# Kernel tuning notes

Measured on AMD Instinct MI355X. Metric: run time of the kernel, lower is better.

Reference implementation:

```python
import jax, jax.numpy as jnp
import numpy as np

DIM, HEADS, FFN, E = 1024, 16, 4096, 8
B, S = 2, 1024
EPS = 1e-5


def _ln(x, g, b):
    mu = jnp.mean(x, axis=-1, keepdims=True)
    var = jnp.mean((x - mu) ** 2, axis=-1, keepdims=True)
    return (x - mu) * jax.lax.rsqrt(var + EPS) * g + b


def setup_inputs() -> dict:
    key = jax.random.key(0)
    ks = jax.random.split(key, 20)
    sd = 0.02
    d, f = DIM, FFN
    return {
        "x": jax.random.normal(ks[0], (B, S, d), jnp.float32),
        "ln1_g": jnp.ones((d,), jnp.float32), "ln1_b": jnp.zeros((d,), jnp.float32),
        "Wqkv": jax.random.normal(ks[1], (d, 3 * d), jnp.float32) * sd,
        "bqkv": jnp.zeros((3 * d,), jnp.float32),
        "Wo": jax.random.normal(ks[2], (d, d), jnp.float32) * sd,
        "bo": jnp.zeros((d,), jnp.float32),
        "ln2_g": jnp.ones((d,), jnp.float32), "ln2_b": jnp.zeros((d,), jnp.float32),
        "gate_w": jax.random.normal(ks[3], (d, E), jnp.float32) * sd,
        "W1": jax.random.normal(ks[4], (E, d, f), jnp.float32) * sd,
        "b1": jnp.zeros((E, f), jnp.float32),
        "W2": jax.random.normal(ks[5], (E, f, d), jnp.float32) * sd,
        "b2": jnp.zeros((E, d), jnp.float32),
        "rW1": jax.random.normal(ks[6], (d, f), jnp.float32) * sd,
        "rb1": jnp.zeros((f,), jnp.float32),
        "rW2": jax.random.normal(ks[7], (f, d), jnp.float32) * sd,
        "rb2": jnp.zeros((d,), jnp.float32),
        "coef_w": jax.random.normal(ks[8], (d, 2), jnp.float32) * sd,
        "coef_b": jnp.zeros((2,), jnp.float32),
    }


def reference(x, ln1_g, ln1_b, Wqkv, bqkv, Wo, bo, ln2_g, ln2_b, gate_w,
              W1, b1, W2, b2, rW1, rb1, rW2, rb2, coef_w, coef_b):
    b, s, d = x.shape
    h, dh = HEADS, d // HEADS

    # --- attention block ---
    xn = _ln(x, ln1_g, ln1_b)
    qkv = xn @ Wqkv + bqkv                       # [b,s,3d]
    q, k, v = jnp.split(qkv, 3, axis=-1)
    q = q.reshape(b, s, h, dh)
    k = k.reshape(b, s, h, dh)
    v = v.reshape(b, s, h, dh)
    scores = jnp.einsum("bqhd,bkhd->bhqk", q, k) / jnp.sqrt(jnp.float32(dh))
    attn = jax.nn.softmax(scores, axis=-1)
    ctx = jnp.einsum("bhqk,bkhd->bqhd", attn, v).reshape(b, s, d)
    x = x + ctx @ Wo + bo

    # --- MoE FFN block (top-1 gating, DeepSpeed residual MoE) ---
    xn2 = _ln(x, ln2_g, ln2_b)
    xt = xn2.reshape(b * s, d)                   # [T,d] tokens
    probs = jax.nn.softmax(xt @ gate_w, axis=-1)  # [T,E]
    gate_val = jnp.max(probs, axis=-1, keepdims=True)   # top-1 prob
    expert_idx = jnp.argmax(probs, axis=-1)
    oh = jax.nn.one_hot(expert_idx, E, dtype=xt.dtype)  # [T,E] dispatch mask

    xe = jnp.einsum("te,td->etd", oh, xt)        # dispatch [E,T,d]
    he = jax.nn.gelu(jnp.einsum("etd,edf->etf", xe, W1) + b1[:, None, :], approximate=False)
    ye = jnp.einsum("etf,efd->etd", he, W2) + b2[:, None, :]
    moe_out = jnp.einsum("te,etd->td", oh, ye) * gate_val  # combine [T,d]

    # residual dense expert + learned mixing coefficient
    rm = jax.nn.gelu(xt @ rW1 + rb1, approximate=False) @ rW2 + rb2
    coef = jax.nn.softmax(xt @ coef_w + coef_b, axis=-1)  # [T,2]
    ff = moe_out * coef[:, 0:1] + rm * coef[:, 1:2]

    return x + ff.reshape(b, s, d)
```

## Files before the change

### kernel.cpp

```cpp
#include <hip/hip_runtime.h>
#include <math.h>

#define TOK 2048
#define NDIM 1024

typedef __attribute__((ext_vector_type(4))) float f32x4;
typedef __attribute__((ext_vector_type(8))) short s16x8;
typedef __attribute__((ext_vector_type(4))) short s16x4;

__device__ __forceinline__ short f2bf(float x) {
  unsigned int u = __builtin_bit_cast(unsigned int, x);
  unsigned int r = (u + 0x7fffu + ((u >> 16) & 1u)) >> 16;
  return (short)r;
}
__device__ __forceinline__ void gload_lds16(const void* g, void* l) {
  __builtin_amdgcn_global_load_lds((const __attribute__((address_space(1))) void*)g,
                                   (__attribute__((address_space(3))) void*)l, 16, 0, 0);
}

struct PackP { const float* src; short* dst; int K, N, nkt; };
__global__ __launch_bounds__(256)
void pack_k(PackP p)
{
  __shared__ short T[64][264];
  const int nkt = p.nkt;
  const int cb = blockIdx.x / nkt, kt = blockIdx.x % nkt;
  const int ntn = p.N >> 7;
  const float* src = p.src + (size_t)blockIdx.y * p.K * p.N + (size_t)(kt * 64) * p.N + cb * 256;
  const int t = threadIdx.x;
  #pragma unroll
  for (int i = 0; i < 16; ++i) {
    const int r = i * 4 + (t >> 6);
    const f32x4 v = *(const f32x4*)(src + (size_t)r * p.N + (t & 63) * 4);
    short* d = &T[r][(t & 63) * 4];
    d[0] = f2bf(v[0]); d[1] = f2bf(v[1]); d[2] = f2bf(v[2]); d[3] = f2bf(v[3]);
  }
  __syncthreads();
  #pragma unroll
  for (int j = 0; j < 2; ++j) {
    short* dst = p.dst + ((size_t)(blockIdx.y * ntn + cb * 2 + j) * nkt + kt) * 8192;
    #pragma unroll
    for (int jj = 0; jj < 4; ++jj) {
      const int ch = t * 4 + jj;
      const int col = ch >> 3, od = ch & 7, o = od ^ (col & 7);
      s16x8 v;
      #pragma unroll
      for (int kk = 0; kk < 8; ++kk) v[kk] = T[o * 8 + kk][j * 128 + col];
      *(s16x8*)(dst + ch * 8) = v;
    }
  }
}

__global__ __launch_bounds__(256)
void ln_k(const float* __restrict__ x, const float* __restrict__ g,
          const float* __restrict__ bb, short* __restrict__ out)
{
  const int row = blockIdx.x, tid = threadIdx.x;
  const f32x4 xv = *(const f32x4*)(x + (size_t)row * NDIM + tid * 4);
  float s = xv[0] + xv[1] + xv[2] + xv[3];
  float s2 = xv[0]*xv[0] + xv[1]*xv[1] + xv[2]*xv[2] + xv[3]*xv[3];
  #pragma unroll
  for (int m = 1; m < 64; m <<= 1) { s += __shfl_xor(s, m); s2 += __shfl_xor(s2, m); }
  __shared__ float red[8];
  const int w = tid >> 6, l = tid & 63;
  if (l == 0) { red[w] = s; red[4 + w] = s2; }
  __syncthreads();
  s = red[0] + red[1] + red[2] + red[3];
  s2 = red[4] + red[5] + red[6] + red[7];
  const float mean = s * (1.0f / NDIM);
  const float var = s2 * (1.0f / NDIM) - mean * mean;
  const float rstd = rsqrtf(var + 1e-5f);
  const f32x4 gv = *(const f32x4*)(g + tid * 4);
  const f32x4 bv = *(const f32x4*)(bb + tid * 4);
  s16x4 ov;
  #pragma unroll
  for (int j = 0; j < 4; ++j) ov[j] = f2bf((xv[j] - mean) * rstd * gv[j] + bv[j]);
  *(s16x4*)(out + (size_t)row * NDIM + tid * 4) = ov;
}

__global__ __launch_bounds__(256)
void gate_k(const float* __restrict__ x1, const float* __restrict__ g,
            const float* __restrict__ bb, const float* __restrict__ gw,
            const float* __restrict__ cw, const float* __restrict__ cb,
            int* __restrict__ counts, int* __restrict__ bucket,
            float* __restrict__ gs, float* __restrict__ c1o)
{
  const int tid = threadIdx.x, l = tid & 63, w = tid >> 6;
  const int t = blockIdx.x * 4 + w;
  f32x4 xv[4];
  #pragma unroll
  for (int it = 0; it < 4; ++it)
    xv[it] = *(const f32x4*)(x1 + (size_t)t * NDIM + it * 256 + l * 4);
  float s = 0.f, s2 = 0.f;
  #pragma unroll
  for (int it = 0; it < 4; ++it)
    #pragma unroll
    for (int j = 0; j < 4; ++j) { s += xv[it][j]; s2 += xv[it][j] * xv[it][j]; }
  #pragma unroll
  for (int m = 1; m < 64; m <<= 1) { s += __shfl_xor(s, m); s2 += __shfl_xor(s2, m); }
  const float mean = s * (1.0f / NDIM);
  const float rstd = rsqrtf(s2 * (1.0f / NDIM) - mean * mean + 1e-5f);
  float acc[10];
  #pragma unroll
  for (int j = 0; j < 10; ++j) acc[j] = 0.f;
  #pragma unroll
  for (int it = 0; it < 4; ++it) {
    #pragma unroll
    for (int j = 0; j < 4; ++j) {
      const int d0 = it * 256 + l * 4 + j;
      const float xn = (xv[it][j] - mean) * rstd * g[d0] + bb[d0];
      const f32x4 g0 = *(const f32x4*)(gw + (size_t)d0 * 8);
      const f32x4 g1 = *(const f32x4*)(gw + (size_t)d0 * 8 + 4);
      #pragma unroll
      for (int q = 0; q < 4; ++q) { acc[q] += xn * g0[q]; acc[4 + q] += xn * g1[q]; }
      acc[8] += xn * cw[d0 * 2]; acc[9] += xn * cw[d0 * 2 + 1];
    }
  }
  #pragma unroll
  for (int j = 0; j < 10; ++j)
    #pragma unroll
    for (int m = 1; m < 64; m <<= 1) acc[j] += __shfl_xor(acc[j], m);
  if (l == 0) {
    int best = 0; float mx = acc[0];
    #pragma unroll
    for (int e = 1; e < 8; ++e) if (acc[e] > mx) { mx = acc[e]; best = e; }
    float se = 0.f;
    #pragma unroll
    for (int e = 0; e < 8; ++e) se += __expf(acc[e] - mx);
    const float gate_val = 1.0f / se;
    const float l0 = acc[8] + cb[0], l1 = acc[9] + cb[1];
    const float cmx = fmaxf(l0, l1);
    const float e0 = __expf(l0 - cmx), e1 = __expf(l1 - cmx);
    const float inv = 1.0f / (e0 + e1);
    const int pos = atomicAdd(&counts[best], 1);
    bucket[best * TOK + pos] = t;
    gs[t] = gate_val * e0 * inv;
    c1o[t] = e1 * inv;
  }
}

struct GemmP {
  const short* A; const short* A2; const short* Bp; const short* Bp2;
  const float* bias; const float* bias2;
  short* outh; short* outh2; float* outf;
  const float* resid; const float* gs; const float* c1;
  const int* bucket; const int* counts;
  int N, K, ktc, nmt;
};

template<int MODE>
__global__ __launch_bounds__(256, 3)
void gemm_k(GemmP p)
{
  __shared__ short Al[8192];
  __shared__ short Bl[8192];
  const int tid = threadIdx.x;
  const int l = tid & 63, w = tid >> 6;
  const int wr = w >> 1, wc = w & 1;
  const int ntn = p.N >> 7, nkt = p.K >> 6;
  const int nwg = p.nmt * ntn;
  const int logical = (blockIdx.x & 7) * (nwg >> 3) + (blockIdx.x >> 3);
  const int nt = logical / p.nmt;
  const int mt = logical % p.nmt;
  const int z = blockIdx.z;
  const bool first = (z == 0);
  const int K = p.K, N = p.N;

  int e = 0, cnt = TOK;
  const int* bucket = nullptr;
  if (MODE >= 2) {
    e = blockIdx.y;
    if (e < 8) {
      cnt = p.counts[e];
      if (mt * 128 >= cnt) return;
      bucket = p.bucket + e * TOK;
    }
  }
  const short* Abase = (MODE == 3 && e == 8) ? p.A2 : p.A;
  const float* bias = (MODE >= 2) ? (e < 8 ? p.bias + (size_t)e * N : p.bias2) : p.bias;
  const short* btile = (MODE >= 2)
      ? (e < 8 ? p.Bp + ((size_t)(e * ntn + nt) * nkt) * 8192
               : p.Bp2 + ((size_t)nt * nkt) * 8192)
      : p.Bp + ((size_t)nt * nkt) * 8192;

  const short* aptr[4];
  #pragma unroll
  for (int i = 0; i < 4; ++i) {
    const int rl = (i * 256 + tid) >> 3;
    int row;
    if (bucket) {
      const int bidx = mt * 128 + rl;
      row = bucket[bidx < cnt ? bidx : mt * 128];
    } else row = mt * 128 + rl;
    aptr[i] = Abase + (size_t)row * K + ((tid & 7) ^ (rl & 7)) * 8;
  }

  const int kt0 = z * p.ktc, kt1 = kt0 + p.ktc;

  f32x4 acc[4][4] = {};
  for (int kt = kt0; kt < kt1; ++kt) {
    const short* bsrc = btile + kt * 8192;
    #pragma unroll
    for (int j = 0; j < 4; ++j)
      gload_lds16(bsrc + (j * 256 + tid) * 8, (char*)Bl + (j * 256 + (tid & 192)) * 16);
    #pragma unroll
    for (int i = 0; i < 4; ++i)
      gload_lds16(aptr[i] + kt * 64, (char*)Al + (i * 256 + (tid & 192)) * 16);
    __syncthreads();
    #pragma unroll
    for (int ks = 0; ks < 2; ++ks) {
      const int octd = (ks * 4 + (l >> 4)) ^ (l & 7);
      s16x8 af[4], bfr[4];
      #pragma unroll
      for (int mf = 0; mf < 4; ++mf)
        af[mf] = *(const s16x8*)((char*)Al +
            (wr * 64 + mf * 16 + (l & 15)) * 128 + octd * 16);
      #pragma unroll
      for (int nf = 0; nf < 4; ++nf)
        bfr[nf] = *(const s16x8*)((char*)Bl +
            (wc * 64 + nf * 16 + (l & 15)) * 128 + octd * 16);
      #pragma unroll
      for (int mf = 0; mf < 4; ++mf)
        #pragma unroll
        for (int nf = 0; nf < 4; ++nf)
          acc[mf][nf] = __builtin_amdgcn_mfma_f32_16x16x32_bf16(af[mf], bfr[nf], acc[mf][nf], 0, 0, 0);
    }
    __syncthreads();
  }

  short* oh = (MODE == 2) ? (e < 8 ? p.outh : p.outh2) : p.outh;
  #pragma unroll
  for (int mf = 0; mf < 4; ++mf) {
    #pragma unroll
    for (int i = 0; i < 4; ++i) {
      const int rloc = wr * 64 + mf * 16 + (l >> 4) * 4 + i;
      int grow; bool valid = true;
      if (bucket) {
        const int bidx = mt * 128 + rloc;
        valid = bidx < cnt;
        grow = valid ? bucket[bidx] : 0;
      } else grow = mt * 128 + rloc;
      float srow = 1.f;
      if (MODE == 3) srow = (e < 8) ? (valid ? p.gs[grow] : 0.f) : p.c1[grow];
      #pragma unroll
      for (int nf = 0; nf < 4; ++nf) {
        const int col = nt * 128 + wc * 64 + nf * 16 + (l & 15);
        const size_t off = (size_t)grow * N + col;
        const float bc = first ? bias[col] : 0.f;
        if (MODE == 0) {
          oh[off] = f2bf(acc[mf][nf][i] + bc);
        } else if (MODE == 1) {
          atomicAdd(&p.outf[off], acc[mf][nf][i] + bc + (first ? p.resid[off] : 0.f));
        } else if (MODE == 2) {
          const float v = acc[mf][nf][i] + bc;
          const float gv = 0.5f * v * (1.0f + erff(v * 0.70710678f));
          if (valid) oh[off] = f2bf(gv);
        } else if (MODE == 3) {
          if (valid)
            atomicAdd(&p.outf[off], (acc[mf][nf][i] + bc) * srow +
                      ((e == 8 && first) ? p.resid[off] : 0.f));
        }
      }
    }
  }
}

__global__ __launch_bounds__(256, 2)
void attn_k(const short* __restrict__ qkv, short* __restrict__ ctx)
{
  __shared__ short Klds[64 * 64];
  __shared__ short Vlds[64 * 64];
  __shared__ short Plds[4 * 16 * 64];
  const int tid = threadIdx.x, l = tid & 63, w = tid >> 6;
  const int qt = blockIdx.x;
  const int bh = blockIdx.y;
  const int b = bh >> 4, h = bh & 15;
  const size_t tbase = (size_t)b * 1024;

  const int sq = qt * 64 + w * 16 + (l & 15);
  s16x8 qf[2];
  #pragma unroll
  for (int ks = 0; ks < 2; ++ks)
    qf[ks] = *(const s16x8*)(qkv + (tbase + sq) * 3072 + h * 64 + ks * 32 + (l >> 4) * 8);

  f32x4 o[4] = {};
  float mrow[4], lrow[4];
  #pragma unroll
  for (int i = 0; i < 4; ++i) { mrow[i] = -1e30f; lrow[i] = 0.f; }

  for (int kt = 0; kt < 16; ++kt) {
    #pragma unroll
    for (int i = 0; i < 2; ++i) {
      const int s = i * 256 + tid;
      const int r = s >> 3, c = s & 7, csrc = c ^ (r & 7);
      const short* gsrc = qkv + (tbase + kt * 64 + r) * 3072 + 1024 + h * 64 + csrc * 8;
      gload_lds16(gsrc, (char*)Klds + (i * 256 + (tid & 192)) * 16);
    }
    #pragma unroll
    for (int i = 0; i < 2; ++i) {
      const int kv0 = (i * 4 + w) * 8;
      s16x8 vv;
      #pragma unroll
      for (int j = 0; j < 8; ++j)
        vv[j] = qkv[(tbase + kt * 64 + kv0 + j) * 3072 + 2048 + h * 64 + l];
      *(s16x8*)((char*)Vlds + ((l * 128 + kv0 * 2) ^ ((l & 7) << 4))) = vv;
    }
    __syncthreads();

    f32x4 sv[4];
    #pragma unroll
    for (int nf = 0; nf < 4; ++nf) {
      f32x4 a = {0.f, 0.f, 0.f, 0.f};
      const int kv = nf * 16 + (l & 15);
      #pragma unroll
      for (int ks = 0; ks < 2; ++ks) {
        const s16x8 kb = *(const s16x8*)((char*)Klds +
            ((kv * 128 + (ks * 32 + (l >> 4) * 8) * 2) ^ ((kv & 7) << 4)));
        a = __builtin_amdgcn_mfma_f32_16x16x32_bf16(qf[ks], kb, a, 0, 0, 0);
      }
      sv[nf] = a * 0.125f;
    }
    float sc[4], ps[4];
    #pragma unroll
    for (int i = 0; i < 4; ++i) {
      float m = fmaxf(fmaxf(sv[0][i], sv[1][i]), fmaxf(sv[2][i], sv[3][i]));
      #pragma unroll
      for (int msk = 1; msk < 16; msk <<= 1) m = fmaxf(m, __shfl_xor(m, msk));
      const float mn = fmaxf(mrow[i], m);
      sc[i] = __expf(mrow[i] - mn);
      mrow[i] = mn;
      ps[i] = 0.f;
    }
    #pragma unroll
    for (int nf = 0; nf < 4; ++nf)
      #pragma unroll
      for (int i = 0; i < 4; ++i) {
        const float pp = __expf(sv[nf][i] - mrow[i]);
        sv[nf][i] = pp;
        ps[i] += pp;
      }
    #pragma unroll
    for (int i = 0; i < 4; ++i) {
      #pragma unroll
      for (int msk = 1; msk < 16; msk <<= 1) ps[i] += __shfl_xor(ps[i], msk);
      lrow[i] = lrow[i] * sc[i] + ps[i];
    }
    #pragma unroll
    for (int nf = 0; nf < 4; ++nf)
      #pragma unroll
      for (int i = 0; i < 4; ++i) o[nf][i] *= sc[i];

    char* pw = (char*)Plds + w * 2048;
    #pragma unroll
    for (int nf = 0; nf < 4; ++nf)
      #pragma unroll
      for (int i = 0; i < 4; ++i) {
        const int q = (l >> 4) * 4 + i;
        *(short*)(pw + ((q * 128 + (nf * 16 + (l & 15)) * 2) ^ ((q & 7) << 4))) = f2bf(sv[nf][i]);
      }
    __syncthreads();
    #pragma unroll
    for (int ks = 0; ks < 2; ++ks) {
      const s16x8 pa = *(const s16x8*)(pw +
          (((l & 15) * 128 + (ks * 32 + (l >> 4) * 8) * 2) ^ ((l & 7) << 4)));
      #pragma unroll
      for (int nf = 0; nf < 4; ++nf) {
        const int dh = nf * 16 + (l & 15);
        const s16x8 vb = *(const s16x8*)((char*)Vlds +
            ((dh * 128 + (ks * 32 + (l >> 4) * 8) * 2) ^ ((dh & 7) << 4)));
        o[nf] = __builtin_amdgcn_mfma_f32_16x16x32_bf16(pa, vb, o[nf], 0, 0, 0);
      }
    }
    __syncthreads();
  }
  #pragma unroll
  for (int i = 0; i < 4; ++i) {
    const float inv = 1.0f / lrow[i];
    const size_t t = tbase + qt * 64 + w * 16 + (l >> 4) * 4 + i;
    #pragma unroll
    for (int nf = 0; nf < 4; ++nf)
      ctx[t * 1024 + h * 64 + nf * 16 + (l & 15)] = f2bf(o[nf][i] * inv);
  }
}

extern "C" void kernel_launch(void* const* d_in, const int* in_sizes, int n_in,
                              void* d_out, int out_size, void* d_ws, size_t ws_size,
                              hipStream_t stream)
{
  const float* x    = (const float*)d_in[0];
  const float* ln1g = (const float*)d_in[1];
  const float* ln1b = (const float*)d_in[2];
  const float* Wqkv = (const float*)d_in[3];
  const float* bqkv = (const float*)d_in[4];
  const float* Wo   = (const float*)d_in[5];
  const float* bo   = (const float*)d_in[6];
  const float* ln2g = (const float*)d_in[7];
  const float* ln2b = (const float*)d_in[8];
  const float* gw   = (const float*)d_in[9];
  const float* W1   = (const float*)d_in[10];
  const float* b1   = (const float*)d_in[11];
  const float* W2   = (const float*)d_in[12];
  const float* b2   = (const float*)d_in[13];
  const float* rW1  = (const float*)d_in[14];
  const float* rb1  = (const float*)d_in[15];
  const float* rW2  = (const float*)d_in[16];
  const float* rb2  = (const float*)d_in[17];
  const float* cw   = (const float*)d_in[18];
  const float* cb   = (const float*)d_in[19];
  float* out = (float*)d_out;

  char* ws = (char*)d_ws;
  const size_t MB = 1024 * 1024;
  short* xn1    = (short*)(ws + 0);
  short* qkv    = (short*)(ws + 4 * MB);
  short* he     = (short*)(ws + 4 * MB);
  short* ctx    = (short*)(ws + 16 * MB);
  float* x1     = (float*)(ws + 20 * MB);
  short* xn2    = (short*)(ws + 28 * MB);
  short* hr     = (short*)(ws + 32 * MB);
  int*   counts = (int*)(ws + 56 * MB);
  int*   bucket = (int*)(ws + 56 * MB + 256);
  float* gs     = (float*)(ws + 56 * MB + 256 + 64 * 1024);
  float* c1     = (float*)(ws + 56 * MB + 256 + 64 * 1024 + 8192);
  short* Wqkvp  = (short*)(ws + 64 * MB);
  short* Wop    = (short*)(ws + 70 * MB);
  short* W1p    = (short*)(ws + 72 * MB);
  short* W2p    = (short*)(ws + 136 * MB);
  short* rW1p   = (short*)(ws + 200 * MB);
  short* rW2p   = (short*)(ws + 208 * MB);

  hipMemsetAsync(counts, 0, 8 * sizeof(int), stream);
  hipMemsetAsync(x1, 0, TOK * NDIM * sizeof(float), stream);
  hipMemsetAsync(out, 0, TOK * NDIM * sizeof(float), stream);

  PackP pk;
  pk = PackP{Wqkv, Wqkvp, 1024, 3072, 16}; pack_k<<<dim3(12 * 16, 1), 256, 0, stream>>>(pk);
  pk = PackP{Wo,   Wop,   1024, 1024, 16}; pack_k<<<dim3(4 * 16, 1), 256, 0, stream>>>(pk);
  pk = PackP{W1,   W1p,   1024, 4096, 16}; pack_k<<<dim3(16 * 16, 8), 256, 0, stream>>>(pk);
  pk = PackP{W2,   W2p,   4096, 1024, 64}; pack_k<<<dim3(4 * 64, 8), 256, 0, stream>>>(pk);
  pk = PackP{rW1,  rW1p,  1024, 4096, 16}; pack_k<<<dim3(16 * 16, 1), 256, 0, stream>>>(pk);
  pk = PackP{rW2,  rW2p,  4096, 1024, 64}; pack_k<<<dim3(4 * 64, 1), 256, 0, stream>>>(pk);

  ln_k<<<TOK, 256, 0, stream>>>(x, ln1g, ln1b, xn1);

  GemmP p{};
  p.A = xn1; p.Bp = Wqkvp; p.bias = bqkv; p.outh = qkv;
  p.N = 3072; p.K = 1024; p.ktc = 16; p.nmt = 16;
  gemm_k<0><<<dim3(384), 256, 0, stream>>>(p);

  attn_k<<<dim3(16, 32), 256, 0, stream>>>(qkv, ctx);

  p = GemmP{};
  p.A = ctx; p.Bp = Wop; p.bias = bo; p.outf = x1; p.resid = x;
  p.N = 1024; p.K = 1024; p.ktc = 8; p.nmt = 16;
  gemm_k<1><<<dim3(128, 1, 2), 256, 0, stream>>>(p);

  ln_k<<<TOK, 256, 0, stream>>>(x1, ln2g, ln2b, xn2);
  gate_k<<<TOK / 4, 256, 0, stream>>>(x1, ln2g, ln2b, gw, cw, cb, counts, bucket, gs, c1);

  p = GemmP{};
  p.A = xn2; p.Bp = W1p; p.Bp2 = rW1p; p.bias = b1; p.bias2 = rb1;
  p.outh = he; p.outh2 = hr; p.N = 4096; p.K = 1024; p.ktc = 16; p.nmt = 16;
  p.bucket = bucket; p.counts = counts;
  gemm_k<2><<<dim3(512, 9), 256, 0, stream>>>(p);

  p = GemmP{};
  p.A = he; p.A2 = hr; p.Bp = W2p; p.Bp2 = rW2p; p.bias = b2; p.bias2 = rb2;
  p.outf = out; p.resid = x1; p.gs = gs; p.c1 = c1;
  p.N = 1024; p.K = 4096; p.ktc = 32; p.nmt = 16;
  p.bucket = bucket; p.counts = counts;
  gemm_k<3><<<dim3(128, 9, 2), 256, 0, stream>>>(p);
}
```

Before: 500.5 us.

## Add 256x256 double-buffered GEMM kernel for MoE expert FFN layers

Adds a new 512-thread GEMM kernel with 256x256 output tiles and double-buffered LDS staging (prefetching the next k-tile while computing the current one) for the expert and residual FFN GEMMs. The weight packing gains a wide 256-column tile format to match. The original kernel is simplified to the dense modes only. The intent is more data reuse per tile and overlap of global loads with MFMA work. The cost is lower occupancy (one block per CU, large LDS), more wasted rows for sparsely filled expert buckets at 256-row granularity, and fewer workgroups overall.

```diff
diff --git a/kernel.cpp b/kernel.cpp
--- a/kernel.cpp
+++ b/kernel.cpp
@@ -18,14 +18,13 @@
                                    (__attribute__((address_space(3))) void*)l, 16, 0, 0);
 }
 
-struct PackP { const float* src; short* dst; int K, N, nkt; };
+struct PackP { const float* src; short* dst; int K, N, nkt, wide; };
 __global__ __launch_bounds__(256)
 void pack_k(PackP p)
 {
   __shared__ short T[64][264];
   const int nkt = p.nkt;
   const int cb = blockIdx.x / nkt, kt = blockIdx.x % nkt;
-  const int ntn = p.N >> 7;
   const float* src = p.src + (size_t)blockIdx.y * p.K * p.N + (size_t)(kt * 64) * p.N + cb * 256;
   const int t = threadIdx.x;
   #pragma unroll
@@ -36,17 +35,32 @@
     d[0] = f2bf(v[0]); d[1] = f2bf(v[1]); d[2] = f2bf(v[2]); d[3] = f2bf(v[3]);
   }
   __syncthreads();
-  #pragma unroll
-  for (int j = 0; j < 2; ++j) {
-    short* dst = p.dst + ((size_t)(blockIdx.y * ntn + cb * 2 + j) * nkt + kt) * 8192;
-    #pragma unroll
-    for (int jj = 0; jj < 4; ++jj) {
-      const int ch = t * 4 + jj;
+  if (p.wide) {
+    const int ntn = p.N >> 8;
+    short* dst = p.dst + ((size_t)(blockIdx.y * ntn + cb) * nkt + kt) * 16384;
+    #pragma unroll
+    for (int jj = 0; jj < 8; ++jj) {
+      const int ch = t * 8 + jj;
       const int col = ch >> 3, od = ch & 7, o = od ^ (col & 7);
       s16x8 v;
       #pragma unroll
-      for (int kk = 0; kk < 8; ++kk) v[kk] = T[o * 8 + kk][j * 128 + col];
+      for (int kk = 0; kk < 8; ++kk) v[kk] = T[o * 8 + kk][col];
       *(s16x8*)(dst + ch * 8) = v;
+    }
+  } else {
+    const int ntn = p.N >> 7;
+    #pragma unroll
+    for (int j = 0; j < 2; ++j) {
+      short* dst = p.dst + ((size_t)(blockIdx.y * ntn + cb * 2 + j) * nkt + kt) * 8192;
+      #pragma unroll
+      for (int jj = 0; jj < 4; ++jj) {
+        const int ch = t * 4 + jj;
+        const int col = ch >> 3, od = ch & 7, o = od ^ (col & 7);
+        s16x8 v;
+        #pragma unroll
+        for (int kk = 0; kk < 8; ++kk) v[kk] = T[o * 8 + kk][j * 128 + col];
+        *(s16x8*)(dst + ch * 8) = v;
+      }
     }
   }
 }
@@ -165,38 +179,18 @@
   const int z = blockIdx.z;
   const bool first = (z == 0);
   const int K = p.K, N = p.N;
-
-  int e = 0, cnt = TOK;
-  const int* bucket = nullptr;
-  if (MODE >= 2) {
-    e = blockIdx.y;
-    if (e < 8) {
-      cnt = p.counts[e];
-      if (mt * 128 >= cnt) return;
-      bucket = p.bucket + e * TOK;
-    }
-  }
-  const short* Abase = (MODE == 3 && e == 8) ? p.A2 : p.A;
-  const float* bias = (MODE >= 2) ? (e < 8 ? p.bias + (size_t)e * N : p.bias2) : p.bias;
-  const short* btile = (MODE >= 2)
-      ? (e < 8 ? p.Bp + ((size_t)(e * ntn + nt) * nkt) * 8192
-               : p.Bp2 + ((size_t)nt * nkt) * 8192)
-      : p.Bp + ((size_t)nt * nkt) * 8192;
+  const short* btile = p.Bp + ((size_t)nt * nkt) * 8192;
+  const float* bias = p.bias;
 
   const short* aptr[4];
   #pragma unroll
   for (int i = 0; i < 4; ++i) {
     const int rl = (i * 256 + tid) >> 3;
-    int row;
-    if (bucket) {
-      const int bidx = mt * 128 + rl;
-      row = bucket[bidx < cnt ? bidx : mt * 128];
-    } else row = mt * 128 + rl;
-    aptr[i] = Abase + (size_t)row * K + ((tid & 7) ^ (rl & 7)) * 8;
+    const int row = mt * 128 + rl;
+    aptr[i] = p.A + (size_t)row * K + ((tid & 7) ^ (rl & 7)) * 8;
   }
 
   const int kt0 = z * p.ktc, kt1 = kt0 + p.ktc;
-
   f32x4 acc[4][4] = {};
   for (int kt = kt0; kt < kt1; ++kt) {
     const short* bsrc = btile + kt * 8192;
@@ -209,16 +203,18 @@
     __syncthreads();
     #pragma unroll
     for (int ks = 0; ks < 2; ++ks) {
-      const int octd = (ks * 4 + (l >> 4)) ^ (l & 7);
+      const int octd0 = ks * 4 + (l >> 4);
       s16x8 af[4], bfr[4];
       #pragma unroll
-      for (int mf = 0; mf < 4; ++mf)
-        af[mf] = *(const s16x8*)((char*)Al +
-            (wr * 64 + mf * 16 + (l & 15)) * 128 + octd * 16);
-      #pragma unroll
-      for (int nf = 0; nf < 4; ++nf)
-        bfr[nf] = *(const s16x8*)((char*)Bl +
-            (wc * 64 + nf * 16 + (l & 15)) * 128 + octd * 16);
+      for (int mf = 0; mf < 4; ++mf) {
+        const int r = wr * 64 + mf * 16 + (l & 15);
+        af[mf] = *(const s16x8*)((char*)Al + r * 128 + (octd0 ^ (r & 7)) * 16);
+      }
+      #pragma unroll
+      for (int nf = 0; nf < 4; ++nf) {
+        const int c2 = wc * 64 + nf * 16 + (l & 15);
+        bfr[nf] = *(const s16x8*)((char*)Bl + c2 * 128 + (octd0 ^ (c2 & 7)) * 16);
+      }
       #pragma unroll
       for (int mf = 0; mf < 4; ++mf)
         #pragma unroll
@@ -228,36 +224,142 @@
     __syncthreads();
   }
 
-  short* oh = (MODE == 2) ? (e < 8 ? p.outh : p.outh2) : p.outh;
   #pragma unroll
   for (int mf = 0; mf < 4; ++mf) {
     #pragma unroll
     for (int i = 0; i < 4; ++i) {
-      const int rloc = wr * 64 + mf * 16 + (l >> 4) * 4 + i;
-      int grow; bool valid = true;
-      if (bucket) {
-        const int bidx = mt * 128 + rloc;
-        valid = bidx < cnt;
-        grow = valid ? bucket[bidx] : 0;
-      } else grow = mt * 128 + rloc;
-      float srow = 1.f;
-      if (MODE == 3) srow = (e < 8) ? (valid ? p.gs[grow] : 0.f) : p.c1[grow];
+      const int grow = mt * 128 + wr * 64 + mf * 16 + (l >> 4) * 4 + i;
       #pragma unroll
       for (int nf = 0; nf < 4; ++nf) {
         const int col = nt * 128 + wc * 64 + nf * 16 + (l & 15);
         const size_t off = (size_t)grow * N + col;
         const float bc = first ? bias[col] : 0.f;
         if (MODE == 0) {
-          oh[off] = f2bf(acc[mf][nf][i] + bc);
-        } else if (MODE == 1) {
+          p.outh[off] = f2bf(acc[mf][nf][i] + bc);
+        } else {
           atomicAdd(&p.outf[off], acc[mf][nf][i] + bc + (first ? p.resid[off] : 0.f));
-        } else if (MODE == 2) {
-          const float v = acc[mf][nf][i] + bc;
+        }
+      }
+    }
+  }
+}
+
+template<int MODE>
+__global__ __launch_bounds__(512, 1)
+void gemm256_k(GemmP p)
+{
+  __shared__ short Al[2][16384];
+  __shared__ short Bl[2][16384];
+  const int tid = threadIdx.x;
+  const int l = tid & 63, wid = tid >> 6;
+  const int wr = wid >> 2, wc = wid & 3;
+  const int ntn = p.N >> 8, nkt = p.K >> 6;
+  const int nwg = p.nmt * ntn;
+  const int logical = (blockIdx.x & 7) * (nwg >> 3) + (blockIdx.x >> 3);
+  const int nt = logical / p.nmt;
+  const int mt = logical % p.nmt;
+  const int z = blockIdx.z;
+  const bool first = (z == 0);
+  const int K = p.K, N = p.N;
+
+  const int e = blockIdx.y;
+  int cnt = TOK;
+  const int* bucket = nullptr;
+  if (e < 8) {
+    cnt = p.counts[e];
+    if (mt * 256 >= cnt) return;
+    bucket = p.bucket + e * TOK;
+  }
+  const short* Abase = (MODE == 3 && e == 8) ? p.A2 : p.A;
+  const float* bias = (e < 8) ? p.bias + (size_t)e * N : p.bias2;
+  const short* btile = (e < 8) ? p.Bp + ((size_t)(e * ntn + nt) * nkt) * 16384
+                               : p.Bp2 + ((size_t)nt * nkt) * 16384;
+
+  const short* aptr[4];
+  #pragma unroll
+  for (int i = 0; i < 4; ++i) {
+    const int rl = (i * 512 + tid) >> 3;
+    int row;
+    if (bucket) {
+      const int bidx = mt * 256 + rl;
+      row = bucket[bidx < cnt ? bidx : mt * 256];
+    } else row = mt * 256 + rl;
+    aptr[i] = Abase + (size_t)row * K + ((tid & 7) ^ (rl & 7)) * 8;
+  }
+
+  auto stage = [&](int kt, int buf) {
+    const short* bsrc = btile + (size_t)kt * 16384;
+    #pragma unroll
+    for (int i = 0; i < 4; ++i)
+      gload_lds16(aptr[i] + kt * 64, (char*)Al[buf] + (i * 512 + (tid & 448)) * 16);
+    #pragma unroll
+    for (int i = 0; i < 4; ++i)
+      gload_lds16(bsrc + (i * 512 + tid) * 8, (char*)Bl[buf] + (i * 512 + (tid & 448)) * 16);
+  };
+
+  const int kt0 = z * p.ktc, kt1 = kt0 + p.ktc;
+  f32x4 acc[8][4] = {};
+  stage(kt0, 0);
+  __syncthreads();
+  for (int kt = kt0; kt < kt1; ++kt) {
+    const int cur = (kt - kt0) & 1;
+    if (kt + 1 < kt1) stage(kt + 1, cur ^ 1);
+    __builtin_amdgcn_s_setprio(1);
+    #pragma unroll
+    for (int ks = 0; ks < 2; ++ks) {
+      const int octd0 = ks * 4 + (l >> 4);
+      s16x8 bfr[4];
+      #pragma unroll
+      for (int nf = 0; nf < 4; ++nf) {
+        const int c2 = wc * 64 + nf * 16 + (l & 15);
+        bfr[nf] = *(const s16x8*)((char*)Bl[cur] + c2 * 128 + (octd0 ^ (c2 & 7)) * 16);
+      }
+      #pragma unroll
+      for (int mfh = 0; mfh < 2; ++mfh) {
+        s16x8 af[4];
+        #pragma unroll
+        for (int mf = 0; mf < 4; ++mf) {
+          const int r = wr * 128 + mfh * 64 + mf * 16 + (l & 15);
+          af[mf] = *(const s16x8*)((char*)Al[cur] + r * 128 + (octd0 ^ (r & 7)) * 16);
+        }
+        #pragma unroll
+        for (int mf = 0; mf < 4; ++mf)
+          #pragma unroll
+          for (int nf = 0; nf < 4; ++nf)
+            acc[mfh * 4 + mf][nf] =
+                __builtin_amdgcn_mfma_f32_16x16x32_bf16(af[mf], bfr[nf], acc[mfh * 4 + mf][nf], 0, 0, 0);
+      }
+    }
+    __builtin_amdgcn_s_setprio(0);
+    __syncthreads();
+  }
+
+  short* oh = (e < 8) ? p.outh : p.outh2;
+  #pragma unroll
+  for (int m8 = 0; m8 < 8; ++m8) {
+    #pragma unroll
+    for (int i = 0; i < 4; ++i) {
+      const int rloc = wr * 128 + (m8 >> 2) * 64 + (m8 & 3) * 16 + (l >> 4) * 4 + i;
+      int grow; bool valid = true;
+      if (bucket) {
+        const int bidx = mt * 256 + rloc;
+        valid = bidx < cnt;
+        grow = valid ? bucket[bidx] : 0;
+      } else grow = mt * 256 + rloc;
+      float srow = 1.f;
+      if (MODE == 3) srow = (e < 8) ? (valid ? p.gs[grow] : 0.f) : p.c1[grow];
+      #pragma unroll
+      for (int nf = 0; nf < 4; ++nf) {
+        const int col = nt * 256 + wc * 64 + nf * 16 + (l & 15);
+        const size_t off = (size_t)grow * N + col;
+        const float bc = first ? bias[col] : 0.f;
+        if (MODE == 2) {
+          const float v = acc[m8][nf][i] + bc;
           const float gv = 0.5f * v * (1.0f + erff(v * 0.70710678f));
           if (valid) oh[off] = f2bf(gv);
-        } else if (MODE == 3) {
+        } else {
           if (valid)
-            atomicAdd(&p.outf[off], (acc[mf][nf][i] + bc) * srow +
+            atomicAdd(&p.outf[off], (acc[m8][nf][i] + bc) * srow +
                       ((e == 8 && first) ? p.resid[off] : 0.f));
         }
       }
@@ -434,12 +536,12 @@
   hipMemsetAsync(out, 0, TOK * NDIM * sizeof(float), stream);
 
   PackP pk;
-  pk = PackP{Wqkv, Wqkvp, 1024, 3072, 16}; pack_k<<<dim3(12 * 16, 1), 256, 0, stream>>>(pk);
-  pk = PackP{Wo,   Wop,   1024, 1024, 16}; pack_k<<<dim3(4 * 16, 1), 256, 0, stream>>>(pk);
-  pk = PackP{W1,   W1p,   1024, 4096, 16}; pack_k<<<dim3(16 * 16, 8), 256, 0, stream>>>(pk);
-  pk = PackP{W2,   W2p,   4096, 1024, 64}; pack_k<<<dim3(4 * 64, 8), 256, 0, stream>>>(pk);
-  pk = PackP{rW1,  rW1p,  1024, 4096, 16}; pack_k<<<dim3(16 * 16, 1), 256, 0, stream>>>(pk);
-  pk = PackP{rW2,  rW2p,  4096, 1024, 64}; pack_k<<<dim3(4 * 64, 1), 256, 0, stream>>>(pk);
+  pk = PackP{Wqkv, Wqkvp, 1024, 3072, 16, 0}; pack_k<<<dim3(12 * 16, 1), 256, 0, stream>>>(pk);
+  pk = PackP{Wo,   Wop,   1024, 1024, 16, 0}; pack_k<<<dim3(4 * 16, 1), 256, 0, stream>>>(pk);
+  pk = PackP{W1,   W1p,   1024, 4096, 16, 1}; pack_k<<<dim3(16 * 16, 8), 256, 0, stream>>>(pk);
+  pk = PackP{W2,   W2p,   4096, 1024, 64, 1}; pack_k<<<dim3(4 * 64, 8), 256, 0, stream>>>(pk);
+  pk = PackP{rW1,  rW1p,  1024, 4096, 16, 1}; pack_k<<<dim3(16 * 16, 1), 256, 0, stream>>>(pk);
+  pk = PackP{rW2,  rW2p,  4096, 1024, 64, 1}; pack_k<<<dim3(4 * 64, 1), 256, 0, stream>>>(pk);
 
   ln_k<<<TOK, 256, 0, stream>>>(x, ln1g, ln1b, xn1);
 
@@ -460,14 +562,14 @@
 
   p = GemmP{};
   p.A = xn2; p.Bp = W1p; p.Bp2 = rW1p; p.bias = b1; p.bias2 = rb1;
-  p.outh = he; p.outh2 = hr; p.N = 4096; p.K = 1024; p.ktc = 16; p.nmt = 16;
+  p.outh = he; p.outh2 = hr; p.N = 4096; p.K = 1024; p.ktc = 16; p.nmt = 8;
   p.bucket = bucket; p.counts = counts;
-  gemm_k<2><<<dim3(512, 9), 256, 0, stream>>>(p);
+  gemm256_k<2><<<dim3(8 * 16, 9), 512, 0, stream>>>(p);
 
   p = GemmP{};
   p.A = he; p.A2 = hr; p.Bp = W2p; p.Bp2 = rW2p; p.bias = b2; p.bias2 = rb2;
   p.outf = out; p.resid = x1; p.gs = gs; p.c1 = c1;
-  p.N = 1024; p.K = 4096; p.ktc = 32; p.nmt = 16;
+  p.N = 1024; p.K = 4096; p.ktc = 16; p.nmt = 8;
   p.bucket = bucket; p.counts = counts;
-  gemm_k<3><<<dim3(128, 9, 2), 256, 0, stream>>>(p);
-}
+  gemm256_k<3><<<dim3(8 * 4, 9, 4), 512, 0, stream>>>(p);
+}
```

Result: slower. 975.3 us (+94.9%).
